# Performance work log

Hardware: AMD Instinct MI355X
Metric: run time of the kernel (lower is better)

The kernel has to match this reference:

```python
import jax, jax.numpy as jnp
import numpy as np

N = 4096      # nodes
F = 128       # input feature dim
HEADS = 8     # attention_num
U = 8         # units per head


def setup_inputs() -> dict:
    key = jax.random.key(0)
    k_a, k_h, k_w, k_al, k_ar = jax.random.split(key, 5)
    A = jax.random.randint(k_a, (N, N), 0, 2).astype(jnp.float32)   # dense 0/1 adjacency
    H = jax.random.normal(k_h, (N, F), dtype=jnp.float32)
    W = jax.random.normal(k_w, (HEADS, F, U), dtype=jnp.float32) * 0.1
    a_left = jax.random.normal(k_al, (HEADS, U), dtype=jnp.float32) * 0.1
    a_right = jax.random.normal(k_ar, (HEADS, U), dtype=jnp.float32) * 0.1
    return {"A": A, "H": H, "W": W, "a_left": a_left, "a_right": a_right}


def reference(A, H, W, a_left, a_right):
    # Per-head attention logits: E[h,i,j] = e_left[h,i] + e_right[h,j]
    e_l = jnp.einsum('nf,hfu,hu->hn', H, W, a_left)    # [HEADS, N]
    e_r = jnp.einsum('nf,hfu,hu->hn', H, W, a_right)   # [HEADS, N]
    E = e_l[:, :, None] + e_r[:, None, :]              # [HEADS, N, N]
    # Faithful to original: denominator uses exp(E * A) (zeros in A -> exp(0)=1)
    denom = jnp.sum(jnp.exp(E * A[None]), axis=-1, keepdims=True)   # [HEADS, N, 1]
    Alpha = jnp.exp(E) / denom * A[None]               # masked attention weights
    # Aggregate then project: elu(Alpha @ H @ W) per head
    out = jax.nn.elu(jnp.einsum('hij,jf,hfu->hiu', Alpha, H, W))    # [HEADS, N, U]
    # is_output_layer=False -> concat heads along feature dim: [N, HEADS*U]
    return jnp.transpose(out, (1, 0, 2)).reshape(H.shape[0], HEADS * U)
```

## Files before the change

### kernel.cpp

```cpp
#include <hip/hip_runtime.h>
#include <hip/hip_bf16.h>

#define NN 4096
#define FF 128
#define NC 80
#define HPAD 136
#define LSTR 84

typedef __attribute__((ext_vector_type(4))) float float4v;
typedef __attribute__((ext_vector_type(4))) unsigned int uint4v;
typedef __attribute__((ext_vector_type(8))) short short8;
typedef __attribute__((ext_vector_type(8))) unsigned short ushort8;
typedef __attribute__((ext_vector_type(4))) unsigned short ushort4v;

static __device__ inline unsigned short bfb(float x) {
    __hip_bfloat16 b = __float2bfloat16(x);
    return *(unsigned short*)&b;
}
static __device__ inline float bff(unsigned short u) {
    __hip_bfloat16 b = *(__hip_bfloat16*)&u;
    return __bfloat162float(b);
}

__global__ __launch_bounds__(128) void gat_prep(const float* __restrict__ H,
                                                const float* __restrict__ W,
                                                const float* __restrict__ al,
                                                const float* __restrict__ ar,
                                                float* __restrict__ expEl,
                                                __hip_bfloat16* __restrict__ Bp)
{
    __shared__ unsigned short Hhi[32 * HPAD], Hlo[32 * HPAD];
    __shared__ unsigned short Whi[16 * NC * 8], Wlo[16 * NC * 8];
    const int t  = threadIdx.x;
    const int j0 = blockIdx.x * 32;

    {
        const int jr = t >> 2, f0 = (t & 3) * 32;
        const float* src = H + (size_t)(j0 + jr) * FF + f0;
        unsigned short* dh = Hhi + jr * HPAD + f0;
        unsigned short* dl = Hlo + jr * HPAD + f0;
        #pragma unroll
        for (int i = 0; i < 32; i += 4) {
            float4v x = *(const float4v*)(src + i);
            ushort4v hv, lv;
            #pragma unroll
            for (int c2 = 0; c2 < 4; ++c2) {
                unsigned short h = bfb(x[c2]);
                hv[c2] = h;
                lv[c2] = bfb(x[c2] - bff(h));
            }
            *(ushort4v*)(dh + i) = hv;
            *(ushort4v*)(dl + i) = lv;
        }
    }
    {
        const int hu = t & 63;
        const int fb = (t >> 6) * 64;
        const float* wsrc = W + (size_t)(hu >> 3) * (FF * 8) + (hu & 7);
        #pragma unroll
        for (int g8 = 0; g8 < 8; ++g8) {
            const int f0 = fb + g8 * 8;
            ushort8 hv, lv;
            #pragma unroll
            for (int i = 0; i < 8; ++i) {
                float x = wsrc[(size_t)(f0 + i) * 8];
                unsigned short h = bfb(x);
                hv[i] = h; lv[i] = bfb(x - bff(h));
            }
            const int g = (f0 >> 5) * 4 + ((f0 >> 3) & 3);
            *(ushort8*)&Whi[((size_t)g * NC + hu) * 8] = hv;
            *(ushort8*)&Wlo[((size_t)g * NC + hu) * 8] = lv;
        }
    }
    {
        const int h  = t >> 4;
        const int f0 = (t & 15) * 8;
        float arv[8], alv[8];
        #pragma unroll
        for (int u = 0; u < 8; ++u) { arv[u] = ar[h * 8 + u]; alv[u] = al[h * 8 + u]; }
        ushort8 rh, rl, lh, ll;
        #pragma unroll
        for (int i = 0; i < 8; ++i) {
            const float* wp = W + (size_t)h * (FF * 8) + (size_t)(f0 + i) * 8;
            float sr = 0.f, sl = 0.f;
            #pragma unroll
            for (int u = 0; u < 8; ++u) { float w = wp[u]; sr += w * arv[u]; sl += w * alv[u]; }
            unsigned short a = bfb(sr); rh[i] = a; rl[i] = bfb(sr - bff(a));
            unsigned short b = bfb(sl); lh[i] = b; ll[i] = bfb(sl - bff(b));
        }
        const int g = (f0 >> 5) * 4 + ((f0 >> 3) & 3);
        *(ushort8*)&Whi[((size_t)g * NC + 64 + h) * 8] = rh;
        *(ushort8*)&Wlo[((size_t)g * NC + 64 + h) * 8] = rl;
        *(ushort8*)&Whi[((size_t)g * NC + 72 + h) * 8] = lh;
        *(ushort8*)&Wlo[((size_t)g * NC + 72 + h) * 8] = ll;
    }
    __syncthreads();

    const int w = t >> 6, lane = t & 63;
    const int m16 = lane & 15, q = lane >> 4;

    float4v acc[5] = {};
    #pragma unroll
    for (int kt = 0; kt < 4; ++kt) {
        short8 ahi = *(const short8*)&Hhi[(w * 16 + m16) * HPAD + kt * 32 + q * 8];
        short8 alo = *(const short8*)&Hlo[(w * 16 + m16) * HPAD + kt * 32 + q * 8];
        #pragma unroll
        for (int nt = 0; nt < 5; ++nt) {
            short8 bhi = *(const short8*)&Whi[((size_t)(kt * 4 + q) * NC + nt * 16 + m16) * 8];
            short8 blo = *(const short8*)&Wlo[((size_t)(kt * 4 + q) * NC + nt * 16 + m16) * 8];
            acc[nt] = __builtin_amdgcn_mfma_f32_16x16x32_bf16(ahi, bhi, acc[nt], 0, 0, 0);
            acc[nt] = __builtin_amdgcn_mfma_f32_16x16x32_bf16(alo, bhi, acc[nt], 0, 0, 0);
            acc[nt] = __builtin_amdgcn_mfma_f32_16x16x32_bf16(ahi, blo, acc[nt], 0, 0, 0);
        }
    }

    const int jbase = j0 + w * 16 + q * 4;
    float ex[4];
    #pragma unroll
    for (int r = 0; r < 4; ++r) ex[r] = expf(acc[4][r]);
    if (m16 >= 8) {
        #pragma unroll
        for (int r = 0; r < 4; ++r)
            expEl[(m16 - 8) * NN + jbase + r] = ex[r];
    }
    #pragma unroll
    for (int r = 0; r < 4; ++r) {
        const int j = jbase + r;
        const size_t base = ((size_t)((j >> 5) * 4 + ((j >> 3) & 3)) * NC) * 8 + (j & 7);
        #pragma unroll
        for (int nt = 0; nt < 4; ++nt) {
            const int srcl = (lane & 48) | (nt * 2 + (m16 >> 3));
            const float er = __shfl(ex[r], srcl);
            Bp[base + (size_t)(nt * 16 + m16) * 8] = __float2bfloat16(er * acc[nt][r]);
        }
        const float v = (m16 < 8) ? ex[r] : (m16 == 8 ? 1.0f : 0.0f);
        Bp[base + (size_t)(64 + m16) * 8] = __float2bfloat16(v);
    }
}

__global__ __launch_bounds__(512) void gat_gemm(const float* __restrict__ A,
                                                const __hip_bfloat16* __restrict__ Bp,
                                                const float* __restrict__ expEl,
                                                float* __restrict__ out)
{
    __shared__ float Ls[8 * 16 * LSTR];
    const int rb   = blockIdx.x;
    const int wave = threadIdx.x >> 6;
    const int lane = threadIdx.x & 63;
    const int m16  = lane & 15;
    const int q    = lane >> 4;
    const int row0 = rb * 16;

    float4v acc[5] = {};

    const int k0 = wave * 512;
    const unsigned int* Au = (const unsigned int*)A;
    const short* Bs = (const short*)Bp;
    const unsigned int* arow = Au + (size_t)(row0 + m16) * NN + q * 8;

    uint4v a0 = *(const uint4v*)(arow + k0);
    uint4v a1 = *(const uint4v*)(arow + k0 + 4);

    #pragma unroll 4
    for (int kt = 0; kt < 16; ++kt) {
        const int kk = k0 + kt * 32;
        short8 afrag;
        afrag[0] = (short)(a0[0] >> 16); afrag[1] = (short)(a0[1] >> 16);
        afrag[2] = (short)(a0[2] >> 16); afrag[3] = (short)(a0[3] >> 16);
        afrag[4] = (short)(a1[0] >> 16); afrag[5] = (short)(a1[1] >> 16);
        afrag[6] = (short)(a1[2] >> 16); afrag[7] = (short)(a1[3] >> 16);

        if (kt + 1 < 16) {
            a0 = *(const uint4v*)(arow + kk + 32);
            a1 = *(const uint4v*)(arow + kk + 36);
        }

        const int ktg = kk >> 5;
        const short8* bbase = (const short8*)(Bs + ((size_t)(ktg * 4 + q) * NC) * 8);
        #pragma unroll
        for (int nt = 0; nt < 5; ++nt) {
            short8 bfrag = bbase[nt * 16 + m16];
            acc[nt] = __builtin_amdgcn_mfma_f32_16x16x32_bf16(afrag, bfrag, acc[nt], 0, 0, 0);
        }
    }

    float* Lw = Ls + wave * (16 * LSTR);
    #pragma unroll
    for (int nt = 0; nt < 5; ++nt) {
        #pragma unroll
        for (int r = 0; r < 4; ++r)
            Lw[(q * 4 + r) * LSTR + nt * 16 + m16] = acc[nt][r];
    }
    __syncthreads();

    #pragma unroll
    for (int p = threadIdx.x; p < 1024; p += 512) {
        const int il = p >> 6;
        const int c  = p & 63;
        const int h  = c >> 3;
        float T = 0.f, S = 0.f, dg = 0.f;
        #pragma unroll
        for (int w = 0; w < 8; ++w) {
            const float* rowp = Ls + w * (16 * LSTR) + il * LSTR;
            T  += rowp[c];
            S  += rowp[64 + h];
            dg += rowp[72];
        }
        const float el = expEl[h * NN + row0 + il];
        const float denom = ((float)NN - dg) + el * S;
        const float x = el * T / denom;
        out[(size_t)(row0 + il) * 64 + c] = x > 0.f ? x : expf(x) - 1.f;
    }
}

extern "C" void kernel_launch(void* const* d_in, const int* in_sizes, int n_in,
                              void* d_out, int out_size, void* d_ws, size_t ws_size,
                              hipStream_t stream) {
    const float* A  = (const float*)d_in[0];
    const float* H  = (const float*)d_in[1];
    const float* W  = (const float*)d_in[2];
    const float* al = (const float*)d_in[3];
    const float* ar = (const float*)d_in[4];
    float* out = (float*)d_out;

    float* expEl = (float*)d_ws;
    __hip_bfloat16* Bp = (__hip_bfloat16*)((char*)d_ws + 131072);

    gat_prep<<<NN / 32, 128, 0, stream>>>(H, W, al, ar, expEl, Bp);
    gat_gemm<<<NN / 16, 512, 0, stream>>>(A, Bp, expEl, out);
}
```

Baseline: 116.0 us.

## Split K across 16 waves per block with double-buffered A prefetch

Doubles the gat_gemm block to 1024 threads so each of 16 waves covers 256 columns of K instead of 512. The A loads are now double-buffered two tiles ahead. The cross-wave reduction goes in two phases: waves 0-7 write to shared memory, then waves 8-15 add into it, followed by one epilogue pass per thread. The goal is more memory-level parallelism when streaming the large fp32 adjacency matrix. In exchange it adds an extra barrier, tighter register limits at 1024 threads, and possibly lower block-level occupancy.

```diff
diff --git a/kernel.cpp b/kernel.cpp
--- a/kernel.cpp
+++ b/kernel.cpp
@@ -138,10 +138,10 @@
     }
 }
 
-__global__ __launch_bounds__(512) void gat_gemm(const float* __restrict__ A,
-                                                const __hip_bfloat16* __restrict__ Bp,
-                                                const float* __restrict__ expEl,
-                                                float* __restrict__ out)
+__global__ __launch_bounds__(1024) void gat_gemm(const float* __restrict__ A,
+                                                 const __hip_bfloat16* __restrict__ Bp,
+                                                 const float* __restrict__ expEl,
+                                                 float* __restrict__ out)
 {
     __shared__ float Ls[8 * 16 * LSTR];
     const int rb   = blockIdx.x;
@@ -153,27 +153,30 @@
 
     float4v acc[5] = {};
 
-    const int k0 = wave * 512;
+    const int k0 = wave * 256;
     const unsigned int* Au = (const unsigned int*)A;
     const short* Bs = (const short*)Bp;
     const unsigned int* arow = Au + (size_t)(row0 + m16) * NN + q * 8;
 
-    uint4v a0 = *(const uint4v*)(arow + k0);
-    uint4v a1 = *(const uint4v*)(arow + k0 + 4);
-
-    #pragma unroll 4
-    for (int kt = 0; kt < 16; ++kt) {
+    uint4v a0[2], a1[2];
+    a0[0] = *(const uint4v*)(arow + k0);
+    a1[0] = *(const uint4v*)(arow + k0 + 4);
+    a0[1] = *(const uint4v*)(arow + k0 + 32);
+    a1[1] = *(const uint4v*)(arow + k0 + 36);
+
+    #pragma unroll
+    for (int kt = 0; kt < 8; ++kt) {
         const int kk = k0 + kt * 32;
+        uint4v ca0 = a0[kt & 1], ca1 = a1[kt & 1];
+        if (kt + 2 < 8) {
+            a0[kt & 1] = *(const uint4v*)(arow + kk + 64);
+            a1[kt & 1] = *(const uint4v*)(arow + kk + 68);
+        }
         short8 afrag;
-        afrag[0] = (short)(a0[0] >> 16); afrag[1] = (short)(a0[1] >> 16);
-        afrag[2] = (short)(a0[2] >> 16); afrag[3] = (short)(a0[3] >> 16);
-        afrag[4] = (short)(a1[0] >> 16); afrag[5] = (short)(a1[1] >> 16);
-        afrag[6] = (short)(a1[2] >> 16); afrag[7] = (short)(a1[3] >> 16);
-
-        if (kt + 1 < 16) {
-            a0 = *(const uint4v*)(arow + kk + 32);
-            a1 = *(const uint4v*)(arow + kk + 36);
-        }
+        afrag[0] = (short)(ca0[0] >> 16); afrag[1] = (short)(ca0[1] >> 16);
+        afrag[2] = (short)(ca0[2] >> 16); afrag[3] = (short)(ca0[3] >> 16);
+        afrag[4] = (short)(ca1[0] >> 16); afrag[5] = (short)(ca1[1] >> 16);
+        afrag[6] = (short)(ca1[2] >> 16); afrag[7] = (short)(ca1[3] >> 16);
 
         const int ktg = kk >> 5;
         const short8* bbase = (const short8*)(Bs + ((size_t)(ktg * 4 + q) * NC) * 8);
@@ -184,19 +187,27 @@
         }
     }
 
-    float* Lw = Ls + wave * (16 * LSTR);
-    #pragma unroll
-    for (int nt = 0; nt < 5; ++nt) {
-        #pragma unroll
-        for (int r = 0; r < 4; ++r)
-            Lw[(q * 4 + r) * LSTR + nt * 16 + m16] = acc[nt][r];
+    float* Lw = Ls + (wave & 7) * (16 * LSTR);
+    if (wave < 8) {
+        #pragma unroll
+        for (int nt = 0; nt < 5; ++nt)
+            #pragma unroll
+            for (int r = 0; r < 4; ++r)
+                Lw[(q * 4 + r) * LSTR + nt * 16 + m16] = acc[nt][r];
     }
     __syncthreads();
-
-    #pragma unroll
-    for (int p = threadIdx.x; p < 1024; p += 512) {
-        const int il = p >> 6;
-        const int c  = p & 63;
+    if (wave >= 8) {
+        #pragma unroll
+        for (int nt = 0; nt < 5; ++nt)
+            #pragma unroll
+            for (int r = 0; r < 4; ++r)
+                Lw[(q * 4 + r) * LSTR + nt * 16 + m16] += acc[nt][r];
+    }
+    __syncthreads();
+
+    {
+        const int il = threadIdx.x >> 6;
+        const int c  = threadIdx.x & 63;
         const int h  = c >> 3;
         float T = 0.f, S = 0.f, dg = 0.f;
         #pragma unroll
@@ -227,5 +238,5 @@
     __hip_bfloat16* Bp = (__hip_bfloat16*)((char*)d_ws + 131072);
 
     gat_prep<<<NN / 32, 128, 0, stream>>>(H, W, al, ar, expEl, Bp);
-    gat_gemm<<<NN / 16, 512, 0, stream>>>(A, Bp, expEl, out);
-}
+    gat_gemm<<<NN / 16, 1024, 0, stream>>>(A, Bp, expEl, out);
+}
```

New measurement: 117.5 us. No clear change (+1.3%).
